# Kernel optimization log

Hardware: AMD Instinct MI355X
Metric: run time of the kernel (lower is better)

## Reference

```python
import jax, jax.numpy as jnp
import numpy as np

N, E, C_IN, HID, K, NLAYERS = 1024, 2048, 4, 192, 5, 4


def setup_inputs() -> dict:
    key = jax.random.key(0)
    ks = jax.random.split(key, 24)
    s = 0.05
    x = jax.random.normal(ks[0], (N, C_IN), jnp.float32)
    src = jax.random.randint(ks[1], (E,), 0, N, dtype=jnp.int32)
    off = jax.random.randint(ks[2], (E,), 1, N, dtype=jnp.int32)
    dst = (src + off) % N  # guarantees no self-loops (ChebConv removes them)
    edge_index = jnp.stack([src, dst])  # [2, E] int32
    edge_attr = jax.random.normal(ks[3], (E, C_IN), jnp.float32)
    batch = jnp.zeros((N,), jnp.int32)  # unused by forward, kept for signature fidelity
    inp = {
        'x': x, 'edge_index': edge_index, 'edge_attr': edge_attr, 'batch': batch,
        # ChebConv(4, 192, K=5): K weight mats + bias
        'cheb_w': jax.random.normal(ks[4], (K, C_IN, HID), jnp.float32) * s,
        'cheb_b': jnp.zeros((HID,), jnp.float32),
        # edge encoder Linear(4, 192)
        'eenc_w': jax.random.normal(ks[5], (C_IN, HID), jnp.float32) * s,
        'eenc_b': jnp.zeros((HID,), jnp.float32),
        # 4 NNConv layers, each with MapE2NxN edge MLP (192->192->192*192),
        # root linear (192x192, no bias) and conv bias
        'nn1_w': jax.random.normal(ks[6], (NLAYERS, HID, HID), jnp.float32) * s,
        'nn1_b': jnp.zeros((NLAYERS, HID), jnp.float32),
        'nn2_w': jax.random.normal(ks[7], (NLAYERS, HID, HID * HID), jnp.float32) * (s / 8.0),
        'nn2_b': jnp.zeros((NLAYERS, HID * HID), jnp.float32),
        'root_w': jax.random.normal(ks[8], (NLAYERS, HID, HID), jnp.float32) * s,
        'conv_b': jnp.zeros((NLAYERS, HID), jnp.float32),
        # LayerNorm per DeepGCNLayer
        'ln_g': jnp.ones((NLAYERS, HID), jnp.float32),
        'ln_b': jnp.zeros((NLAYERS, HID), jnp.float32),
        # final Linear(192, 2)
        'out_w': jax.random.normal(ks[9], (HID, 2), jnp.float32) * s,
        'out_b': jnp.zeros((2,), jnp.float32),
    }
    return inp


def _layernorm(v, g, b):
    mu = jnp.mean(v, axis=-1, keepdims=True)
    var = jnp.mean(jnp.square(v - mu), axis=-1, keepdims=True)
    return (v - mu) * jax.lax.rsqrt(var + 1e-5) * g + b


def reference(x, edge_index, edge_attr, batch, cheb_w, cheb_b, eenc_w, eenc_b,
              nn1_w, nn1_b, nn2_w, nn2_b, root_w, conv_b, ln_g, ln_b, out_w, out_b):
    n = x.shape[0]
    src, dst = edge_index[0], edge_index[1]

    # ---- ChebConv (sym norm, lambda_max=2.0) => L_hat = -D^{-1/2} A D^{-1/2} ----
    deg = jax.ops.segment_sum(jnp.ones_like(src, dtype=x.dtype), src, num_segments=n)
    dinv = jnp.where(deg > 0, 1.0 / jnp.sqrt(jnp.maximum(deg, 1.0)), 0.0)
    wnorm = -dinv[src] * dinv[dst]  # [E]

    def lap(v):  # y = L_hat @ v : gather -> weight -> scatter-add
        return jax.ops.segment_sum(wnorm[:, None] * v[src], dst, num_segments=n)

    Tx0 = x
    out = Tx0 @ cheb_w[0]
    Tx1 = lap(Tx0)
    out = out + Tx1 @ cheb_w[1]
    for k in range(2, K):  # Chebyshev recurrence
        Tx2 = 2.0 * lap(Tx1) - Tx0
        out = out + Tx2 @ cheb_w[k]
        Tx0, Tx1 = Tx1, Tx2
    h = out + cheb_b  # [N, HID]

    # ---- edge encoder ----
    ea = edge_attr @ eenc_w + eenc_b  # [E, HID]

    # ---- NNConv: per-edge MLP-generated weight, gather->edge-GEMM->scatter ----
    def nnconv(v, i):
        theta = (ea @ nn1_w[i] + nn1_b[i]) @ nn2_w[i] + nn2_b[i]  # [E, HID*HID]
        theta = theta.reshape(E, HID, HID)
        msg = jnp.einsum('ei,eio->eo', v[src], theta)  # per-edge matvec
        agg = jax.ops.segment_sum(msg, dst, num_segments=n)  # aggr='add'
        return agg + v @ root_w[i] + conv_b[i]

    # layers[0].conv applied directly (no pre-norm/act)
    h = nnconv(h, 0)
    # layers[1:4] are DeepGCNLayer res+: x + conv(dropout(act(norm(x))))
    for i in range(1, NLAYERS):
        z = jax.nn.relu(_layernorm(h, ln_g[i], ln_b[i]))
        h = h + nnconv(z, i)
    # final: act(layers[0].norm(x)), dropout (eval=identity), linear
    h = jax.nn.relu(_layernorm(h, ln_g[0], ln_b[0]))
    return h @ out_w + out_b  # [N, 2]
```

## Files before the change

kernel.cpp:

```cpp
#include <hip/hip_runtime.h>
#include <stdint.h>

typedef _Float16 half8 __attribute__((ext_vector_type(8)));
typedef float f32x4 __attribute__((ext_vector_type(4)));

typedef const __attribute__((address_space(1))) void* gptr_t;
typedef __attribute__((address_space(3))) void* lptr_t;
static __device__ __forceinline__ void gll16(const void* g, void* l) {
  __builtin_amdgcn_global_load_lds((gptr_t)(unsigned long long)g,
                                   (lptr_t)(unsigned int)(unsigned long long)l,
                                   16, 0, 0);
}

__global__ __launch_bounds__(1024)
void k_chebM(const float* __restrict__ x, const int* __restrict__ ei,
             const float* __restrict__ eenc_w, const float* __restrict__ eenc_b,
             const float* __restrict__ nn1_w, const float* __restrict__ nn1_b,
             float* __restrict__ Tx, float* __restrict__ Mbuf) {
  if (blockIdx.x == 0) {
    __shared__ float deg[1024];
    __shared__ float wn[2048];
    __shared__ float T0[4096], T1[4096], yv[4096];
    int t = threadIdx.x;
    deg[t] = 0.f;
    __syncthreads();
    atomicAdd(&deg[ei[t]], 1.f);
    atomicAdd(&deg[ei[1024 + t]], 1.f);
    __syncthreads();
    for (int e = t; e < 2048; e += 1024) {
      int s = ei[e], d = ei[2048 + e];
      float ds = deg[s], dd = deg[d];
      float a = ds > 0.f ? 1.f / sqrtf(fmaxf(ds, 1.f)) : 0.f;
      float b = dd > 0.f ? 1.f / sqrtf(fmaxf(dd, 1.f)) : 0.f;
      wn[e] = -a * b;
    }
    float4 xv = ((const float4*)x)[t];
    ((float4*)T0)[t] = xv;
    ((float4*)Tx)[t] = xv;
    __syncthreads();
    float* cur = T0; float* nxt = T1;
    for (int rec = 0; rec < 4; ++rec) {
      ((float4*)yv)[t] = make_float4(0.f, 0.f, 0.f, 0.f);
      __syncthreads();
      for (int e = t; e < 2048; e += 1024) {
        int s = ei[e], d = ei[2048 + e];
        float wv = wn[e];
#pragma unroll
        for (int c = 0; c < 4; ++c) atomicAdd(&yv[d * 4 + c], wv * cur[s * 4 + c]);
      }
      __syncthreads();
      float a = (rec == 0) ? 1.f : 2.f;
      float4 y4 = ((float4*)yv)[t];
      float4 p4 = ((float4*)nxt)[t];
      float4 n4;
      n4.x = a * y4.x - (rec ? p4.x : 0.f);
      n4.y = a * y4.y - (rec ? p4.y : 0.f);
      n4.z = a * y4.z - (rec ? p4.z : 0.f);
      n4.w = a * y4.w - (rec ? p4.w : 0.f);
      ((float4*)nxt)[t] = n4;
      ((float4*)(Tx + (rec + 1) * 4096))[t] = n4;
      __syncthreads();
      float* tmp = cur; cur = nxt; nxt = tmp;
    }
  } else {
    int l = blockIdx.x - 1;
    int t = threadIdx.x;
    if (t < 192) {
      float a0 = 0.f, a1 = 0.f, a2 = 0.f, a3 = 0.f, a4 = 0.f;
      const float* nw = nn1_w + (size_t)l * 36864 + t;
      for (int k = 0; k < 192; ++k) {
        float nv = nw[(size_t)k * 192];
        a0 += eenc_w[k] * nv;
        a1 += eenc_w[192 + k] * nv;
        a2 += eenc_w[384 + k] * nv;
        a3 += eenc_w[576 + k] * nv;
        a4 += eenc_b[k] * nv;
      }
      float* Ml = Mbuf + l * 960;
      Ml[t] = a0; Ml[192 + t] = a1; Ml[384 + t] = a2; Ml[576 + t] = a3;
      Ml[768 + t] = a4 + nn1_b[l * 192 + t];
    }
  }
}

__global__ void k_cheb_out(const float* __restrict__ Tx, const float* __restrict__ cw,
                           const float* __restrict__ cb, float* __restrict__ h) {
  int n = blockIdx.x, o = threadIdx.x;
  float acc = cb[o];
#pragma unroll
  for (int k = 0; k < 5; ++k)
#pragma unroll
    for (int c = 0; c < 4; ++c)
      acc += Tx[k * 4096 + n * 4 + c] * cw[(k * 4 + c) * 192 + o];
  h[n * 192 + o] = acc;
}

__global__ __launch_bounds__(256)
void k_pb(const float* __restrict__ nn2_w, const float* __restrict__ Mbuf,
          float* __restrict__ Ppart) {
  int l = blockIdx.y, kc = blockIdx.z;
  int col = blockIdx.x * 1024 + threadIdx.x * 4;
  const float* W = nn2_w + (size_t)l * 7077888 + col;
  const float* Mp = Mbuf + l * 960 + kc * 96;
  f32x4 acc0 = {}, acc1 = {}, acc2 = {}, acc3 = {}, acc4 = {};
  const size_t rs = 36864;
  const float* Wk = W + (size_t)(kc * 96) * rs;
#pragma unroll 8
  for (int k = 0; k < 96; ++k) {
    f32x4 wv = *(const f32x4*)(Wk + (size_t)k * rs);
    acc0 += wv * Mp[k];
    acc1 += wv * Mp[192 + k];
    acc2 += wv * Mp[384 + k];
    acc3 += wv * Mp[576 + k];
    acc4 += wv * Mp[768 + k];
  }
  float* Pp = Ppart + ((size_t)(kc * 4 + l) * 5) * 36864 + col;
  *(f32x4*)(Pp) = acc0;
  *(f32x4*)(Pp + 36864) = acc1;
  *(f32x4*)(Pp + 2 * 36864) = acc2;
  *(f32x4*)(Pp + 3 * 36864) = acc3;
  *(f32x4*)(Pp + 4 * 36864) = acc4;
}

__global__ void k_stageB(const float* __restrict__ Ppart, const float* __restrict__ nn2_b,
                         const float* __restrict__ root_w, _Float16* __restrict__ Btl) {
  int ck = blockIdx.x, l = blockIdx.y, t = threadIdx.x;
  _Float16* out = Btl + (size_t)l * 221184 + ck * 9216;
#pragma unroll
  for (int it = 0; it < 5; ++it) {
    int n = it * 256 + t;
    if (n >= 1152) break;
    union { _Float16 h[8]; uint4 v; } u;
    if (n < 960) {
      int c = n / 192, o = n - c * 192;
      const float* P0 = Ppart + ((size_t)(0 * 4 + l) * 5 + c) * 36864;
      const float* P1 = Ppart + ((size_t)(1 * 4 + l) * 5 + c) * 36864;
#pragma unroll
      for (int j = 0; j < 8; ++j) {
        int io = (ck * 8 + j) * 192 + o;
        float val = P0[io] + P1[io];
        if (c == 4) val += nn2_b[(size_t)l * 36864 + io];
        u.h[j] = (_Float16)val;
      }
    } else {
      int o = n - 960;
#pragma unroll
      for (int j = 0; j < 8; ++j)
        u.h[j] = (_Float16)root_w[(size_t)l * 36864 + (ck * 8 + j) * 192 + o];
    }
    *(uint4*)(out + (size_t)n * 8) = u.v;
  }
}

__global__ __launch_bounds__(256, 2)
void k_y(const float* __restrict__ z, const _Float16* __restrict__ Btl,
         float* __restrict__ Y, float* __restrict__ agg, int layer) {
  extern __shared__ _Float16 sm[];
  _Float16* Al = sm;
  _Float16* Bl = sm + 24576;
  int t = threadIdx.x;
  int w = t >> 6, lane = t & 63, l15 = lane & 15, q4 = lane >> 4;
  int e0 = blockIdx.x * 128;
  int nb = blockIdx.y;
  const _Float16* Bt = Btl + (size_t)layer * 221184;

  {
    int base4 = (blockIdx.y * 8 + blockIdx.x) * 1024;
    float4 zf = make_float4(0.f, 0.f, 0.f, 0.f);
#pragma unroll
    for (int q = 0; q < 4; ++q) ((float4*)agg)[base4 + q * 256 + t] = zf;
  }
  {
    const char* g = (const char*)Bt + (((size_t)w * 1152 + nb * 192) * 8) * 2;
    char* lb = (char*)Bl + w * 3072;
#pragma unroll
    for (int r = 0; r < 3; ++r) gll16(g + r * 1024 + lane * 16, lb + r * 1024 + lane * 16);
  }
#pragma unroll
  for (int it = 0; it < 12; ++it) {
    int u = it * 256 + t;
    int row = u / 24, ck = u - row * 24;
    const float* ap = z + (size_t)(e0 + row) * 192 + ck * 8;
    float4 v0 = *(const float4*)ap;
    float4 v1 = *(const float4*)(ap + 4);
    union { _Float16 h[8]; uint4 v; } uu;
    uu.h[0] = (_Float16)v0.x; uu.h[1] = (_Float16)v0.y;
    uu.h[2] = (_Float16)v0.z; uu.h[3] = (_Float16)v0.w;
    uu.h[4] = (_Float16)v1.x; uu.h[5] = (_Float16)v1.y;
    uu.h[6] = (_Float16)v1.z; uu.h[7] = (_Float16)v1.w;
    *(uint4*)(Al + ((size_t)ck * 128 + row) * 8) = uu.v;
  }
  __syncthreads();

  f32x4 acc[2][12] = {};
  int buf = 0;
  for (int ks = 0; ks < 6; ++ks) {
    if (ks < 5) {
      const char* g = (const char*)Bt + (((size_t)((ks + 1) * 4 + w) * 1152 + nb * 192) * 8) * 2;
      char* lb = (char*)Bl + (buf ^ 1) * 12288 + w * 3072;
#pragma unroll
      for (int r = 0; r < 3; ++r) gll16(g + r * 1024 + lane * 16, lb + r * 1024 + lane * 16);
    }
    half8 av[2];
#pragma unroll
    for (int mt = 0; mt < 2; ++mt)
      av[mt] = *(const half8*)(Al + (((ks * 4 + q4) * 128) + w * 32 + mt * 16 + l15) * 8);
#pragma unroll
    for (int nt = 0; nt < 12; ++nt) {
      half8 bv = *(const half8*)(Bl + buf * 6144 + ((q4 * 192) + nt * 16 + l15) * 8);
#pragma unroll
      for (int mt = 0; mt < 2; ++mt)
        acc[mt][nt] = __builtin_amdgcn_mfma_f32_16x16x32_f16(av[mt], bv, acc[mt][nt], 0, 0, 0);
    }
    __syncthreads();
    buf ^= 1;
  }
#pragma unroll
  for (int mt = 0; mt < 2; ++mt)
#pragma unroll
    for (int nt = 0; nt < 12; ++nt) {
      int col = nt * 16 + l15;
#pragma unroll
      for (int r = 0; r < 4; ++r) {
        int row = e0 + w * 32 + mt * 16 + q4 * 4 + r;
        Y[(size_t)row * 1152 + nb * 192 + col] = acc[mt][nt][r];
      }
    }
}

__global__ void k_scatter(const int* __restrict__ ei, const float* __restrict__ eattr,
                          const float* __restrict__ Y, float* __restrict__ agg) {
  int o = threadIdx.x;
  int e0 = blockIdx.x * 8;
#pragma unroll
  for (int q = 0; q < 8; ++q) {
    int e = e0 + q;
    int s = ei[e], d = ei[2048 + e];
    const float* yr = Y + (size_t)s * 1152;
    float u0 = eattr[e * 4], u1 = eattr[e * 4 + 1];
    float u2 = eattr[e * 4 + 2], u3 = eattr[e * 4 + 3];
    float m = yr[o] * u0 + yr[192 + o] * u1 + yr[384 + o] * u2 + yr[576 + o] * u3 + yr[768 + o];
    atomicAdd(&agg[(size_t)d * 192 + o], m);
  }
}

__global__ void k_node(const float* __restrict__ hprev, const float* __restrict__ agg,
                       const float* __restrict__ Y, const float* __restrict__ cb,
                       const float* __restrict__ lg, const float* __restrict__ lb,
                       float* __restrict__ hnext, float* __restrict__ znext, int res) {
  __shared__ float r1[192], r2[192];
  __shared__ float mus, vars;
  int n = blockIdx.x, t = threadIdx.x;
  float v = agg[n * 192 + t] + Y[(size_t)n * 1152 + 960 + t] + cb[t];
  if (res) v += hprev[n * 192 + t];
  hnext[n * 192 + t] = v;
  r1[t] = v; r2[t] = v * v;
  __syncthreads();
  if (t < 96) { r1[t] += r1[t + 96]; r2[t] += r2[t + 96]; } __syncthreads();
  if (t < 48) { r1[t] += r1[t + 48]; r2[t] += r2[t + 48]; } __syncthreads();
  if (t < 24) { r1[t] += r1[t + 24]; r2[t] += r2[t + 24]; } __syncthreads();
  if (t < 12) { r1[t] += r1[t + 12]; r2[t] += r2[t + 12]; } __syncthreads();
  if (t < 6)  { r1[t] += r1[t + 6];  r2[t] += r2[t + 6];  } __syncthreads();
  if (t == 0) {
    float s1 = r1[0] + r1[1] + r1[2] + r1[3] + r1[4] + r1[5];
    float s2 = r2[0] + r2[1] + r2[2] + r2[3] + r2[4] + r2[5];
    float mu = s1 / 192.f;
    mus = mu; vars = s2 / 192.f - mu * mu;
  }
  __syncthreads();
  float o = (v - mus) * rsqrtf(vars + 1e-5f) * lg[t] + lb[t];
  znext[n * 192 + t] = fmaxf(o, 0.f);
}

__global__ void k_final(const float* __restrict__ z, const float* __restrict__ ow,
                        const float* __restrict__ ob, float* __restrict__ outp) {
  int t = blockIdx.x * 256 + threadIdx.x;
  if (t >= 2048) return;
  int n = t >> 1, c = t & 1;
  float acc = ob[c];
#pragma unroll 8
  for (int j = 0; j < 192; ++j) acc += z[n * 192 + j] * ow[j * 2 + c];
  outp[t] = acc;
}

extern "C" void kernel_launch(void* const* d_in, const int* in_sizes, int n_in,
                              void* d_out, int out_size, void* d_ws, size_t ws_size,
                              hipStream_t stream) {
  const float* x      = (const float*)d_in[0];
  const int*   ei     = (const int*)  d_in[1];
  const float* eattr  = (const float*)d_in[2];
  const float* cheb_w = (const float*)d_in[4];
  const float* cheb_b = (const float*)d_in[5];
  const float* eenc_w = (const float*)d_in[6];
  const float* eenc_b = (const float*)d_in[7];
  const float* nn1_w  = (const float*)d_in[8];
  const float* nn1_b  = (const float*)d_in[9];
  const float* nn2_w  = (const float*)d_in[10];
  const float* nn2_b  = (const float*)d_in[11];
  const float* root_w = (const float*)d_in[12];
  const float* conv_b = (const float*)d_in[13];
  const float* ln_g   = (const float*)d_in[14];
  const float* ln_bb  = (const float*)d_in[15];
  const float* out_w  = (const float*)d_in[16];
  const float* out_b  = (const float*)d_in[17];
  float* outp = (float*)d_out;
  (void)in_sizes; (void)n_in; (void)out_size; (void)ws_size;

  char* p = (char*)d_ws;
  _Float16* Btl = (_Float16*)p; p += (size_t)4 * 221184 * 2;
  float* Ppart  = (float*)p;    p += (size_t)2 * 4 * 5 * 36864 * 4;
  float* Mbuf   = (float*)p;    p += 4 * 5 * 192 * 4;
  float* Tx     = (float*)p;    p += 5 * 4096 * 4;
  float* Y      = (float*)p;    p += (size_t)1024 * 1152 * 4;
  float* h      = (float*)p;    p += 196608 * 4;
  float* hA     = (float*)p;    p += 196608 * 4;
  float* hB     = (float*)p;    p += 196608 * 4;
  float* zA     = (float*)p;    p += 196608 * 4;
  float* zB     = (float*)p;    p += 196608 * 4;
  float* agg    = (float*)p;    p += 196608 * 4;

  hipFuncSetAttribute(reinterpret_cast<const void*>(&k_y),
                      hipFuncAttributeMaxDynamicSharedMemorySize, 73728);

  k_chebM<<<5, 1024, 0, stream>>>(x, ei, eenc_w, eenc_b, nn1_w, nn1_b, Tx, Mbuf);
  k_cheb_out<<<1024, 192, 0, stream>>>(Tx, cheb_w, cheb_b, h);
  k_pb<<<dim3(36, 4, 2), 256, 0, stream>>>(nn2_w, Mbuf, Ppart);
  k_stageB<<<dim3(24, 4), 256, 0, stream>>>(Ppart, nn2_b, root_w, Btl);

  float* zcur = h;
  float* hcur = h;
  float* hbufs[2] = {hA, hB};
  float* zbufs[2] = {zA, zB};
  for (int l = 0; l < 4; ++l) {
    k_y<<<dim3(8, 6), 256, 73728, stream>>>(zcur, Btl, Y, agg, l);
    k_scatter<<<256, 192, 0, stream>>>(ei, eattr, Y, agg);
    const float* lg = ln_g + (size_t)((l == 3) ? 0 : (l + 1)) * 192;
    const float* lb = ln_bb + (size_t)((l == 3) ? 0 : (l + 1)) * 192;
    k_node<<<1024, 192, 0, stream>>>(hcur, agg, Y, conv_b + (size_t)l * 192,
                                     lg, lb, hbufs[l & 1], zbufs[l & 1], (l == 0) ? 0 : 1);
    hcur = hbufs[l & 1];
    zcur = zbufs[l & 1];
  }
  k_final<<<8, 256, 0, stream>>>(zcur, out_w, out_b, outp);
}
```

Baseline: 342.8 us.

## Fuse per-layer kernels into one cooperative persistent kernel with CSR gather aggregation

Replaces the sequence of per-layer launches (k_y, k_scatter, k_node, k_final, k_stageB, k_cheb_out) with one cooperative kernel of 256 blocks that uses grid syncs between phases. The atomic scatter into agg is replaced by a CSR gather: a dst-sorted edge order is built inside an extra block of k_pb. The Chebyshev recurrence also moves into an idle block of k_pb so it overlaps the large nn2 reduction. The goal is to remove launch overhead, the zeroing of agg and the atomics. The cost is grid-wide barriers, fewer edge rows per MFMA block (64 instead of 128), and serial per-node gather loops.

```diff
diff --git a/kernel.cpp b/kernel.cpp
--- a/kernel.cpp
+++ b/kernel.cpp
@@ -1,5 +1,8 @@
 #include <hip/hip_runtime.h>
+#include <hip/hip_cooperative_groups.h>
 #include <stdint.h>
+
+namespace cg = cooperative_groups;
 
 typedef _Float16 half8 __attribute__((ext_vector_type(8)));
 typedef float f32x4 __attribute__((ext_vector_type(4)));
@@ -12,92 +15,120 @@
                                    16, 0, 0);
 }
 
-__global__ __launch_bounds__(1024)
-void k_chebM(const float* __restrict__ x, const int* __restrict__ ei,
-             const float* __restrict__ eenc_w, const float* __restrict__ eenc_b,
-             const float* __restrict__ nn1_w, const float* __restrict__ nn1_b,
-             float* __restrict__ Tx, float* __restrict__ Mbuf) {
-  if (blockIdx.x == 0) {
-    __shared__ float deg[1024];
-    __shared__ float wn[2048];
-    __shared__ float T0[4096], T1[4096], yv[4096];
-    int t = threadIdx.x;
-    deg[t] = 0.f;
-    __syncthreads();
-    atomicAdd(&deg[ei[t]], 1.f);
-    atomicAdd(&deg[ei[1024 + t]], 1.f);
-    __syncthreads();
-    for (int e = t; e < 2048; e += 1024) {
-      int s = ei[e], d = ei[2048 + e];
-      float ds = deg[s], dd = deg[d];
-      float a = ds > 0.f ? 1.f / sqrtf(fmaxf(ds, 1.f)) : 0.f;
-      float b = dd > 0.f ? 1.f / sqrtf(fmaxf(dd, 1.f)) : 0.f;
-      wn[e] = -a * b;
-    }
-    float4 xv = ((const float4*)x)[t];
-    ((float4*)T0)[t] = xv;
-    ((float4*)Tx)[t] = xv;
-    __syncthreads();
-    float* cur = T0; float* nxt = T1;
-    for (int rec = 0; rec < 4; ++rec) {
-      ((float4*)yv)[t] = make_float4(0.f, 0.f, 0.f, 0.f);
-      __syncthreads();
-      for (int e = t; e < 2048; e += 1024) {
-        int s = ei[e], d = ei[2048 + e];
-        float wv = wn[e];
-#pragma unroll
-        for (int c = 0; c < 4; ++c) atomicAdd(&yv[d * 4 + c], wv * cur[s * 4 + c]);
-      }
-      __syncthreads();
-      float a = (rec == 0) ? 1.f : 2.f;
-      float4 y4 = ((float4*)yv)[t];
-      float4 p4 = ((float4*)nxt)[t];
-      float4 n4;
-      n4.x = a * y4.x - (rec ? p4.x : 0.f);
-      n4.y = a * y4.y - (rec ? p4.y : 0.f);
-      n4.z = a * y4.z - (rec ? p4.z : 0.f);
-      n4.w = a * y4.w - (rec ? p4.w : 0.f);
-      ((float4*)nxt)[t] = n4;
-      ((float4*)(Tx + (rec + 1) * 4096))[t] = n4;
-      __syncthreads();
-      float* tmp = cur; cur = nxt; nxt = tmp;
-    }
-  } else {
-    int l = blockIdx.x - 1;
-    int t = threadIdx.x;
-    if (t < 192) {
-      float a0 = 0.f, a1 = 0.f, a2 = 0.f, a3 = 0.f, a4 = 0.f;
-      const float* nw = nn1_w + (size_t)l * 36864 + t;
-      for (int k = 0; k < 192; ++k) {
-        float nv = nw[(size_t)k * 192];
-        a0 += eenc_w[k] * nv;
-        a1 += eenc_w[192 + k] * nv;
-        a2 += eenc_w[384 + k] * nv;
-        a3 += eenc_w[576 + k] * nv;
-        a4 += eenc_b[k] * nv;
-      }
-      float* Ml = Mbuf + l * 960;
-      Ml[t] = a0; Ml[192 + t] = a1; Ml[384 + t] = a2; Ml[576 + t] = a3;
-      Ml[768 + t] = a4 + nn1_b[l * 192 + t];
-    }
-  }
-}
-
-__global__ void k_cheb_out(const float* __restrict__ Tx, const float* __restrict__ cw,
-                           const float* __restrict__ cb, float* __restrict__ h) {
-  int n = blockIdx.x, o = threadIdx.x;
-  float acc = cb[o];
-#pragma unroll
-  for (int k = 0; k < 5; ++k)
-#pragma unroll
-    for (int c = 0; c < 4; ++c)
-      acc += Tx[k * 4096 + n * 4 + c] * cw[(k * 4 + c) * 192 + o];
-  h[n * 192 + o] = acc;
+__global__ __launch_bounds__(256)
+void k_M(const float* __restrict__ eenc_w, const float* __restrict__ eenc_b,
+         const float* __restrict__ nn1_w, const float* __restrict__ nn1_b,
+         float* __restrict__ Mbuf) {
+  int l = blockIdx.x, t = threadIdx.x;
+  if (t >= 192) return;
+  float a0 = 0.f, a1 = 0.f, a2 = 0.f, a3 = 0.f, a4 = 0.f;
+  const float* nw = nn1_w + (size_t)l * 36864 + t;
+  for (int k = 0; k < 192; ++k) {
+    float nv = nw[(size_t)k * 192];
+    a0 += eenc_w[k] * nv;
+    a1 += eenc_w[192 + k] * nv;
+    a2 += eenc_w[384 + k] * nv;
+    a3 += eenc_w[576 + k] * nv;
+    a4 += eenc_b[k] * nv;
+  }
+  float* Ml = Mbuf + l * 960;
+  Ml[t] = a0; Ml[192 + t] = a1; Ml[384 + t] = a2; Ml[576 + t] = a3;
+  Ml[768 + t] = a4 + nn1_b[l * 192 + t];
 }
 
 __global__ __launch_bounds__(256)
 void k_pb(const float* __restrict__ nn2_w, const float* __restrict__ Mbuf,
-          float* __restrict__ Ppart) {
+          float* __restrict__ Ppart,
+          const float* __restrict__ x, const int* __restrict__ ei,
+          float* __restrict__ Tx, int* __restrict__ rowptr, int* __restrict__ eord) {
+  __shared__ __align__(16) float smem[15360];
+  if (blockIdx.x == 36) {
+    int t = threadIdx.x;
+    if (blockIdx.y == 0 && blockIdx.z == 0) {
+      float* deg = smem;
+      float* wn  = smem + 1024;
+      float* T0  = smem + 3072;
+      float* T1  = smem + 7168;
+      float* yv  = smem + 11264;
+      for (int i = t; i < 1024; i += 256) deg[i] = 0.f;
+      __syncthreads();
+      for (int e = t; e < 2048; e += 256) atomicAdd(&deg[ei[e]], 1.f);
+      __syncthreads();
+      for (int e = t; e < 2048; e += 256) {
+        int s = ei[e], d = ei[2048 + e];
+        float ds = deg[s], dd = deg[d];
+        float a = ds > 0.f ? 1.f / sqrtf(fmaxf(ds, 1.f)) : 0.f;
+        float b = dd > 0.f ? 1.f / sqrtf(fmaxf(dd, 1.f)) : 0.f;
+        wn[e] = -a * b;
+      }
+      for (int i = t; i < 1024; i += 256) {
+        float4 xv = ((const float4*)x)[i];
+        ((float4*)T0)[i] = xv;
+        ((float4*)Tx)[i] = xv;
+      }
+      __syncthreads();
+      float* cur = T0; float* nxt = T1;
+      for (int rec = 0; rec < 4; ++rec) {
+        for (int i = t; i < 1024; i += 256) ((float4*)yv)[i] = make_float4(0.f, 0.f, 0.f, 0.f);
+        __syncthreads();
+        for (int e = t; e < 2048; e += 256) {
+          int s = ei[e], d = ei[2048 + e];
+          float wv = wn[e];
+#pragma unroll
+          for (int c = 0; c < 4; ++c) atomicAdd(&yv[d * 4 + c], wv * cur[s * 4 + c]);
+        }
+        __syncthreads();
+        float a = (rec == 0) ? 1.f : 2.f;
+        for (int i = t; i < 1024; i += 256) {
+          float4 y4 = ((float4*)yv)[i];
+          float4 p4 = ((float4*)nxt)[i];
+          float4 n4;
+          n4.x = a * y4.x - (rec ? p4.x : 0.f);
+          n4.y = a * y4.y - (rec ? p4.y : 0.f);
+          n4.z = a * y4.z - (rec ? p4.z : 0.f);
+          n4.w = a * y4.w - (rec ? p4.w : 0.f);
+          ((float4*)nxt)[i] = n4;
+          ((float4*)(Tx + (rec + 1) * 4096))[i] = n4;
+        }
+        __syncthreads();
+        float* tmp = cur; cur = nxt; nxt = tmp;
+      }
+    } else if (blockIdx.y == 1 && blockIdx.z == 0) {
+      int* cnt = (int*)smem;
+      int* rp  = (int*)(smem + 1024);
+      int* wtot = (int*)(smem + 2048);
+      int lane = t & 63, wv = t >> 6;
+      for (int i = t; i < 1024; i += 256) cnt[i] = 0;
+      __syncthreads();
+      for (int e = t; e < 2048; e += 256) atomicAdd(&cnt[ei[2048 + e]], 1);
+      __syncthreads();
+      int c0 = cnt[t * 4], c1 = cnt[t * 4 + 1], c2 = cnt[t * 4 + 2], c3 = cnt[t * 4 + 3];
+      int s = c0 + c1 + c2 + c3;
+      int inc = s;
+#pragma unroll
+      for (int off = 1; off < 64; off <<= 1) {
+        int u = __shfl_up(inc, off);
+        if (lane >= off) inc += u;
+      }
+      if (lane == 63) wtot[wv] = inc;
+      __syncthreads();
+      int woff = 0;
+#pragma unroll
+      for (int j = 0; j < 4; ++j) if (j < wv) woff += wtot[j];
+      int excl = woff + inc - s;
+      int4 r4; r4.x = excl; r4.y = excl + c0; r4.z = excl + c0 + c1; r4.w = excl + c0 + c1 + c2;
+      *(int4*)(rowptr + t * 4) = r4;
+      if (t == 0) rowptr[1024] = 2048;
+      rp[t * 4] = r4.x; rp[t * 4 + 1] = r4.y; rp[t * 4 + 2] = r4.z; rp[t * 4 + 3] = r4.w;
+      __syncthreads();
+      for (int e = t; e < 2048; e += 256) {
+        int d = ei[2048 + e];
+        int slot = atomicAdd(&rp[d], 1);
+        eord[slot] = e;
+      }
+    }
+    return;
+  }
   int l = blockIdx.y, kc = blockIdx.z;
   int col = blockIdx.x * 1024 + threadIdx.x * 4;
   const float* W = nn2_w + (size_t)l * 7077888 + col;
@@ -122,165 +153,186 @@
   *(f32x4*)(Pp + 4 * 36864) = acc4;
 }
 
-__global__ void k_stageB(const float* __restrict__ Ppart, const float* __restrict__ nn2_b,
-                         const float* __restrict__ root_w, _Float16* __restrict__ Btl) {
-  int ck = blockIdx.x, l = blockIdx.y, t = threadIdx.x;
-  _Float16* out = Btl + (size_t)l * 221184 + ck * 9216;
-#pragma unroll
-  for (int it = 0; it < 5; ++it) {
-    int n = it * 256 + t;
-    if (n >= 1152) break;
-    union { _Float16 h[8]; uint4 v; } u;
-    if (n < 960) {
-      int c = n / 192, o = n - c * 192;
-      const float* P0 = Ppart + ((size_t)(0 * 4 + l) * 5 + c) * 36864;
-      const float* P1 = Ppart + ((size_t)(1 * 4 + l) * 5 + c) * 36864;
-#pragma unroll
-      for (int j = 0; j < 8; ++j) {
-        int io = (ck * 8 + j) * 192 + o;
-        float val = P0[io] + P1[io];
-        if (c == 4) val += nn2_b[(size_t)l * 36864 + io];
-        u.h[j] = (_Float16)val;
-      }
-    } else {
-      int o = n - 960;
-#pragma unroll
-      for (int j = 0; j < 8; ++j)
-        u.h[j] = (_Float16)root_w[(size_t)l * 36864 + (ck * 8 + j) * 192 + o];
-    }
-    *(uint4*)(out + (size_t)n * 8) = u.v;
-  }
-}
-
-__global__ __launch_bounds__(256, 2)
-void k_y(const float* __restrict__ z, const _Float16* __restrict__ Btl,
-         float* __restrict__ Y, float* __restrict__ agg, int layer) {
-  extern __shared__ _Float16 sm[];
+__global__ __launch_bounds__(256)
+void k_all(const float* __restrict__ Ppart, const float* __restrict__ nn2_b,
+           const float* __restrict__ root_w, _Float16* __restrict__ Btl,
+           const float* __restrict__ Tx, const float* __restrict__ cheb_w,
+           const float* __restrict__ cheb_b, float* __restrict__ h0,
+           const int* __restrict__ ei, const float* __restrict__ eattr,
+           const int* __restrict__ rowptr, const int* __restrict__ eord,
+           const float* __restrict__ conv_b, const float* __restrict__ ln_g,
+           const float* __restrict__ ln_b, const float* __restrict__ out_w,
+           const float* __restrict__ out_b,
+           float* __restrict__ Y, float* __restrict__ hA, float* __restrict__ hB,
+           float* __restrict__ zA, float* __restrict__ zB, float* __restrict__ outp) {
+  cg::grid_group grid = cg::this_grid();
+  __shared__ __align__(16) _Float16 sm[24576];
   _Float16* Al = sm;
-  _Float16* Bl = sm + 24576;
-  int t = threadIdx.x;
+  _Float16* Bl = sm + 12288;
+  int b = blockIdx.x, t = threadIdx.x;
   int w = t >> 6, lane = t & 63, l15 = lane & 15, q4 = lane >> 4;
-  int e0 = blockIdx.x * 128;
-  int nb = blockIdx.y;
-  const _Float16* Bt = Btl + (size_t)layer * 221184;
-
+  int n = b * 4 + w;
+  int o0 = lane, o1 = lane + 64, o2 = lane + 128;
+
+  if (b < 96) {
+    int ck = b % 24, l = b / 24;
+    _Float16* out = Btl + (size_t)l * 221184 + ck * 9216;
+#pragma unroll
+    for (int it = 0; it < 5; ++it) {
+      int nn = it * 256 + t;
+      if (nn >= 1152) break;
+      union { _Float16 h[8]; uint4 v; } u;
+      if (nn < 960) {
+        int c = nn / 192, o = nn - c * 192;
+        const float* P0 = Ppart + ((size_t)(0 * 4 + l) * 5 + c) * 36864;
+        const float* P1 = Ppart + ((size_t)(1 * 4 + l) * 5 + c) * 36864;
+#pragma unroll
+        for (int j = 0; j < 8; ++j) {
+          int io = (ck * 8 + j) * 192 + o;
+          float val = P0[io] + P1[io];
+          if (c == 4) val += nn2_b[(size_t)l * 36864 + io];
+          u.h[j] = (_Float16)val;
+        }
+      } else {
+        int o = nn - 960;
+#pragma unroll
+        for (int j = 0; j < 8; ++j)
+          u.h[j] = (_Float16)root_w[(size_t)l * 36864 + (ck * 8 + j) * 192 + o];
+      }
+      *(uint4*)(out + (size_t)nn * 8) = u.v;
+    }
+  }
   {
-    int base4 = (blockIdx.y * 8 + blockIdx.x) * 1024;
-    float4 zf = make_float4(0.f, 0.f, 0.f, 0.f);
-#pragma unroll
-    for (int q = 0; q < 4; ++q) ((float4*)agg)[base4 + q * 256 + t] = zf;
+    float a0 = cheb_b[o0], a1 = cheb_b[o1], a2 = cheb_b[o2];
+#pragma unroll
+    for (int k = 0; k < 5; ++k)
+#pragma unroll
+      for (int c = 0; c < 4; ++c) {
+        float tv = Tx[k * 4096 + n * 4 + c];
+        const float* cwp = cheb_w + (k * 4 + c) * 192;
+        a0 += tv * cwp[o0]; a1 += tv * cwp[o1]; a2 += tv * cwp[o2];
+      }
+    h0[n * 192 + o0] = a0; h0[n * 192 + o1] = a1; h0[n * 192 + o2] = a2;
+  }
+  __threadfence(); grid.sync(); __threadfence();
+
+#pragma unroll
+  for (int l = 0; l < 4; ++l) {
+    const float* zc = (l == 0) ? h0 : ((l == 1) ? zA : ((l == 2) ? zB : zA));
+    float* zo = (l & 1) ? zB : zA;
+    float* ho = (l & 1) ? hB : hA;
+    const float* hp = (l == 2) ? hB : hA;
+    if (b < 96) {
+      int rb = b / 6, cb = b % 6;
+      int e0 = rb * 64;
+      const _Float16* Bt = Btl + (size_t)l * 221184;
+      {
+        const char* g = (const char*)Bt + (((size_t)w * 1152 + cb * 192) * 8) * 2;
+        char* lb = (char*)Bl + w * 3072;
+#pragma unroll
+        for (int r = 0; r < 3; ++r) gll16(g + r * 1024 + lane * 16, lb + r * 1024 + lane * 16);
+      }
+#pragma unroll
+      for (int it = 0; it < 6; ++it) {
+        int u = it * 256 + t;
+        int row = u / 24, ck = u - row * 24;
+        const float* ap = zc + (size_t)(e0 + row) * 192 + ck * 8;
+        float4 v0 = *(const float4*)ap;
+        float4 v1 = *(const float4*)(ap + 4);
+        union { _Float16 h[8]; uint4 v; } uu;
+        uu.h[0] = (_Float16)v0.x; uu.h[1] = (_Float16)v0.y;
+        uu.h[2] = (_Float16)v0.z; uu.h[3] = (_Float16)v0.w;
+        uu.h[4] = (_Float16)v1.x; uu.h[5] = (_Float16)v1.y;
+        uu.h[6] = (_Float16)v1.z; uu.h[7] = (_Float16)v1.w;
+        *(uint4*)(Al + ((size_t)ck * 64 + row) * 8) = uu.v;
+      }
+      __syncthreads();
+      f32x4 acc[12] = {};
+      int buf = 0;
+      for (int ks = 0; ks < 6; ++ks) {
+        if (ks < 5) {
+          const char* g = (const char*)Bt + (((size_t)((ks + 1) * 4 + w) * 1152 + cb * 192) * 8) * 2;
+          char* lb = (char*)Bl + (buf ^ 1) * 12288 + w * 3072;
+#pragma unroll
+          for (int r = 0; r < 3; ++r) gll16(g + r * 1024 + lane * 16, lb + r * 1024 + lane * 16);
+        }
+        half8 av = *(const half8*)(Al + (((ks * 4 + q4) * 64) + w * 16 + l15) * 8);
+#pragma unroll
+        for (int nt = 0; nt < 12; ++nt) {
+          half8 bv = *(const half8*)(Bl + (size_t)buf * 6144 + ((q4 * 192) + nt * 16 + l15) * 8);
+          acc[nt] = __builtin_amdgcn_mfma_f32_16x16x32_f16(av, bv, acc[nt], 0, 0, 0);
+        }
+        __syncthreads();
+        buf ^= 1;
+      }
+#pragma unroll
+      for (int nt = 0; nt < 12; ++nt) {
+        int col = cb * 192 + nt * 16 + l15;
+#pragma unroll
+        for (int r = 0; r < 4; ++r) {
+          int row = e0 + w * 16 + q4 * 4 + r;
+          Y[(size_t)row * 1152 + col] = acc[nt][r];
+        }
+      }
+    }
+    __threadfence(); grid.sync(); __threadfence();
+    {
+      float v0 = 0.f, v1 = 0.f, v2 = 0.f;
+      int beg = rowptr[n], end = rowptr[n + 1];
+      for (int idx = beg; idx < end; ++idx) {
+        int e = eord[idx];
+        int s = ei[e];
+        float4 u = ((const float4*)eattr)[e];
+        const float* yr = Y + (size_t)s * 1152;
+        v0 += yr[o0] * u.x + yr[192 + o0] * u.y + yr[384 + o0] * u.z + yr[576 + o0] * u.w + yr[768 + o0];
+        v1 += yr[o1] * u.x + yr[192 + o1] * u.y + yr[384 + o1] * u.z + yr[576 + o1] * u.w + yr[768 + o1];
+        v2 += yr[o2] * u.x + yr[192 + o2] * u.y + yr[384 + o2] * u.z + yr[576 + o2] * u.w + yr[768 + o2];
+      }
+      const float* yn = Y + (size_t)n * 1152 + 960;
+      const float* cbv = conv_b + l * 192;
+      v0 += yn[o0] + cbv[o0]; v1 += yn[o1] + cbv[o1]; v2 += yn[o2] + cbv[o2];
+      if (l > 0) {
+        v0 += hp[n * 192 + o0]; v1 += hp[n * 192 + o1]; v2 += hp[n * 192 + o2];
+      }
+      ho[n * 192 + o0] = v0; ho[n * 192 + o1] = v1; ho[n * 192 + o2] = v2;
+      float s1 = v0 + v1 + v2, s2 = v0 * v0 + v1 * v1 + v2 * v2;
+#pragma unroll
+      for (int off = 32; off >= 1; off >>= 1) {
+        s1 += __shfl_xor(s1, off);
+        s2 += __shfl_xor(s2, off);
+      }
+      float mu = s1 * (1.f / 192.f);
+      float var = s2 * (1.f / 192.f) - mu * mu;
+      float rcp = rsqrtf(var + 1e-5f);
+      int gi = (l == 3) ? 0 : (l + 1);
+      const float* gg = ln_g + gi * 192;
+      const float* bb = ln_b + gi * 192;
+      zo[n * 192 + o0] = fmaxf((v0 - mu) * rcp * gg[o0] + bb[o0], 0.f);
+      zo[n * 192 + o1] = fmaxf((v1 - mu) * rcp * gg[o1] + bb[o1], 0.f);
+      zo[n * 192 + o2] = fmaxf((v2 - mu) * rcp * gg[o2] + bb[o2], 0.f);
+    }
+    __threadfence(); grid.sync(); __threadfence();
   }
   {
-    const char* g = (const char*)Bt + (((size_t)w * 1152 + nb * 192) * 8) * 2;
-    char* lb = (char*)Bl + w * 3072;
-#pragma unroll
-    for (int r = 0; r < 3; ++r) gll16(g + r * 1024 + lane * 16, lb + r * 1024 + lane * 16);
-  }
-#pragma unroll
-  for (int it = 0; it < 12; ++it) {
-    int u = it * 256 + t;
-    int row = u / 24, ck = u - row * 24;
-    const float* ap = z + (size_t)(e0 + row) * 192 + ck * 8;
-    float4 v0 = *(const float4*)ap;
-    float4 v1 = *(const float4*)(ap + 4);
-    union { _Float16 h[8]; uint4 v; } uu;
-    uu.h[0] = (_Float16)v0.x; uu.h[1] = (_Float16)v0.y;
-    uu.h[2] = (_Float16)v0.z; uu.h[3] = (_Float16)v0.w;
-    uu.h[4] = (_Float16)v1.x; uu.h[5] = (_Float16)v1.y;
-    uu.h[6] = (_Float16)v1.z; uu.h[7] = (_Float16)v1.w;
-    *(uint4*)(Al + ((size_t)ck * 128 + row) * 8) = uu.v;
-  }
-  __syncthreads();
-
-  f32x4 acc[2][12] = {};
-  int buf = 0;
-  for (int ks = 0; ks < 6; ++ks) {
-    if (ks < 5) {
-      const char* g = (const char*)Bt + (((size_t)((ks + 1) * 4 + w) * 1152 + nb * 192) * 8) * 2;
-      char* lb = (char*)Bl + (buf ^ 1) * 12288 + w * 3072;
-#pragma unroll
-      for (int r = 0; r < 3; ++r) gll16(g + r * 1024 + lane * 16, lb + r * 1024 + lane * 16);
-    }
-    half8 av[2];
-#pragma unroll
-    for (int mt = 0; mt < 2; ++mt)
-      av[mt] = *(const half8*)(Al + (((ks * 4 + q4) * 128) + w * 32 + mt * 16 + l15) * 8);
-#pragma unroll
-    for (int nt = 0; nt < 12; ++nt) {
-      half8 bv = *(const half8*)(Bl + buf * 6144 + ((q4 * 192) + nt * 16 + l15) * 8);
-#pragma unroll
-      for (int mt = 0; mt < 2; ++mt)
-        acc[mt][nt] = __builtin_amdgcn_mfma_f32_16x16x32_f16(av[mt], bv, acc[mt][nt], 0, 0, 0);
-    }
-    __syncthreads();
-    buf ^= 1;
-  }
-#pragma unroll
-  for (int mt = 0; mt < 2; ++mt)
-#pragma unroll
-    for (int nt = 0; nt < 12; ++nt) {
-      int col = nt * 16 + l15;
-#pragma unroll
-      for (int r = 0; r < 4; ++r) {
-        int row = e0 + w * 32 + mt * 16 + q4 * 4 + r;
-        Y[(size_t)row * 1152 + nb * 192 + col] = acc[mt][nt][r];
-      }
-    }
-}
-
-__global__ void k_scatter(const int* __restrict__ ei, const float* __restrict__ eattr,
-                          const float* __restrict__ Y, float* __restrict__ agg) {
-  int o = threadIdx.x;
-  int e0 = blockIdx.x * 8;
-#pragma unroll
-  for (int q = 0; q < 8; ++q) {
-    int e = e0 + q;
-    int s = ei[e], d = ei[2048 + e];
-    const float* yr = Y + (size_t)s * 1152;
-    float u0 = eattr[e * 4], u1 = eattr[e * 4 + 1];
-    float u2 = eattr[e * 4 + 2], u3 = eattr[e * 4 + 3];
-    float m = yr[o] * u0 + yr[192 + o] * u1 + yr[384 + o] * u2 + yr[576 + o] * u3 + yr[768 + o];
-    atomicAdd(&agg[(size_t)d * 192 + o], m);
-  }
-}
-
-__global__ void k_node(const float* __restrict__ hprev, const float* __restrict__ agg,
-                       const float* __restrict__ Y, const float* __restrict__ cb,
-                       const float* __restrict__ lg, const float* __restrict__ lb,
-                       float* __restrict__ hnext, float* __restrict__ znext, int res) {
-  __shared__ float r1[192], r2[192];
-  __shared__ float mus, vars;
-  int n = blockIdx.x, t = threadIdx.x;
-  float v = agg[n * 192 + t] + Y[(size_t)n * 1152 + 960 + t] + cb[t];
-  if (res) v += hprev[n * 192 + t];
-  hnext[n * 192 + t] = v;
-  r1[t] = v; r2[t] = v * v;
-  __syncthreads();
-  if (t < 96) { r1[t] += r1[t + 96]; r2[t] += r2[t + 96]; } __syncthreads();
-  if (t < 48) { r1[t] += r1[t + 48]; r2[t] += r2[t + 48]; } __syncthreads();
-  if (t < 24) { r1[t] += r1[t + 24]; r2[t] += r2[t + 24]; } __syncthreads();
-  if (t < 12) { r1[t] += r1[t + 12]; r2[t] += r2[t + 12]; } __syncthreads();
-  if (t < 6)  { r1[t] += r1[t + 6];  r2[t] += r2[t + 6];  } __syncthreads();
-  if (t == 0) {
-    float s1 = r1[0] + r1[1] + r1[2] + r1[3] + r1[4] + r1[5];
-    float s2 = r2[0] + r2[1] + r2[2] + r2[3] + r2[4] + r2[5];
-    float mu = s1 / 192.f;
-    mus = mu; vars = s2 / 192.f - mu * mu;
-  }
-  __syncthreads();
-  float o = (v - mus) * rsqrtf(vars + 1e-5f) * lg[t] + lb[t];
-  znext[n * 192 + t] = fmaxf(o, 0.f);
-}
-
-__global__ void k_final(const float* __restrict__ z, const float* __restrict__ ow,
-                        const float* __restrict__ ob, float* __restrict__ outp) {
-  int t = blockIdx.x * 256 + threadIdx.x;
-  if (t >= 2048) return;
-  int n = t >> 1, c = t & 1;
-  float acc = ob[c];
-#pragma unroll 8
-  for (int j = 0; j < 192; ++j) acc += z[n * 192 + j] * ow[j * 2 + c];
-  outp[t] = acc;
+    const float* zp = zB + (size_t)n * 192;
+    float a0 = 0.f, a1 = 0.f;
+#pragma unroll
+    for (int j = 0; j < 3; ++j) {
+      int k = lane + j * 64;
+      float zk = zp[k];
+      a0 += zk * out_w[k * 2];
+      a1 += zk * out_w[k * 2 + 1];
+    }
+#pragma unroll
+    for (int off = 32; off >= 1; off >>= 1) {
+      a0 += __shfl_xor(a0, off);
+      a1 += __shfl_xor(a1, off);
+    }
+    if (lane == 0) {
+      outp[n * 2] = a0 + out_b[0];
+      outp[n * 2 + 1] = a1 + out_b[1];
+    }
+  }
 }
 
 extern "C" void kernel_launch(void* const* d_in, const int* in_sizes, int n_in,
@@ -312,34 +364,32 @@
   float* Mbuf   = (float*)p;    p += 4 * 5 * 192 * 4;
   float* Tx     = (float*)p;    p += 5 * 4096 * 4;
   float* Y      = (float*)p;    p += (size_t)1024 * 1152 * 4;
-  float* h      = (float*)p;    p += 196608 * 4;
+  float* h0     = (float*)p;    p += 196608 * 4;
   float* hA     = (float*)p;    p += 196608 * 4;
   float* hB     = (float*)p;    p += 196608 * 4;
   float* zA     = (float*)p;    p += 196608 * 4;
   float* zB     = (float*)p;    p += 196608 * 4;
-  float* agg    = (float*)p;    p += 196608 * 4;
-
-  hipFuncSetAttribute(reinterpret_cast<const void*>(&k_y),
-                      hipFuncAttributeMaxDynamicSharedMemorySize, 73728);
-
-  k_chebM<<<5, 1024, 0, stream>>>(x, ei, eenc_w, eenc_b, nn1_w, nn1_b, Tx, Mbuf);
-  k_cheb_out<<<1024, 192, 0, stream>>>(Tx, cheb_w, cheb_b, h);
-  k_pb<<<dim3(36, 4, 2), 256, 0, stream>>>(nn2_w, Mbuf, Ppart);
-  k_stageB<<<dim3(24, 4), 256, 0, stream>>>(Ppart, nn2_b, root_w, Btl);
-
-  float* zcur = h;
-  float* hcur = h;
-  float* hbufs[2] = {hA, hB};
-  float* zbufs[2] = {zA, zB};
-  for (int l = 0; l < 4; ++l) {
-    k_y<<<dim3(8, 6), 256, 73728, stream>>>(zcur, Btl, Y, agg, l);
-    k_scatter<<<256, 192, 0, stream>>>(ei, eattr, Y, agg);
-    const float* lg = ln_g + (size_t)((l == 3) ? 0 : (l + 1)) * 192;
-    const float* lb = ln_bb + (size_t)((l == 3) ? 0 : (l + 1)) * 192;
-    k_node<<<1024, 192, 0, stream>>>(hcur, agg, Y, conv_b + (size_t)l * 192,
-                                     lg, lb, hbufs[l & 1], zbufs[l & 1], (l == 0) ? 0 : 1);
-    hcur = hbufs[l & 1];
-    zcur = zbufs[l & 1];
-  }
-  k_final<<<8, 256, 0, stream>>>(zcur, out_w, out_b, outp);
-}
+  int* rowptr   = (int*)p;      p += 1056 * 4;
+  int* eord     = (int*)p;      p += 2048 * 4;
+
+  k_M<<<4, 256, 0, stream>>>(eenc_w, eenc_b, nn1_w, nn1_b, Mbuf);
+  k_pb<<<dim3(37, 4, 2), 256, 0, stream>>>(nn2_w, Mbuf, Ppart, x, ei, Tx, rowptr, eord);
+
+  const float* a_Pp = Ppart; const float* a_n2b = nn2_b; const float* a_rw = root_w;
+  _Float16* a_Btl = Btl; const float* a_Tx = Tx; const float* a_cw = cheb_w;
+  const float* a_cb = cheb_b; float* a_h0 = h0; const int* a_ei = ei;
+  const float* a_ea = eattr; const int* a_rp = rowptr; const int* a_eo = eord;
+  const float* a_cvb = conv_b; const float* a_lg = ln_g; const float* a_lb = ln_bb;
+  const float* a_ow = out_w; const float* a_ob = out_b; float* a_Y = Y;
+  float* a_hA = hA; float* a_hB = hB; float* a_zA = zA; float* a_zB = zB;
+  float* a_out = outp;
+  void* kargs[] = {
+    (void*)&a_Pp, (void*)&a_n2b, (void*)&a_rw, (void*)&a_Btl, (void*)&a_Tx,
+    (void*)&a_cw, (void*)&a_cb, (void*)&a_h0, (void*)&a_ei, (void*)&a_ea,
+    (void*)&a_rp, (void*)&a_eo, (void*)&a_cvb, (void*)&a_lg, (void*)&a_lb,
+    (void*)&a_ow, (void*)&a_ob, (void*)&a_Y, (void*)&a_hA, (void*)&a_hB,
+    (void*)&a_zA, (void*)&a_zB, (void*)&a_out
+  };
+  hipLaunchCooperativeKernel((const void*)k_all, dim3(256, 1, 1), dim3(256, 1, 1),
+                             kargs, 0u, stream);
+}
```

After: 1.001 ms. +192.1%, slower.
